# Performance work log

Measured on AMD Instinct MI355X. Metric: run time of the kernel, lower is better.

## Reference

```python
import jax, jax.numpy as jnp
import numpy as np

B, P, C, NOBJ = 64, 24564, 81, 16
THRESHOLD = 0.5
NEG_POS_RATIO = 3
ALPHA = 1.0


def cxcy_to_xy(cxcy):
    # (cx, cy, w, h) -> (x_min, y_min, x_max, y_max)
    return jnp.concatenate([cxcy[..., :2] - cxcy[..., 2:] / 2,
                            cxcy[..., :2] + cxcy[..., 2:] / 2], axis=-1)


def xy_to_cxcy(xy):
    return jnp.concatenate([(xy[..., :2] + xy[..., 2:]) / 2,
                            xy[..., 2:] - xy[..., :2]], axis=-1)


def cxcy_to_gcxgcy(cxcy, priors_cxcy):
    # SSD encoding with variances (10, 5)
    g_cxcy = (cxcy[..., :2] - priors_cxcy[..., :2]) / (priors_cxcy[..., 2:] / 10.0)
    g_wh = jnp.log(cxcy[..., 2:] / priors_cxcy[..., 2:]) * 5.0
    return jnp.concatenate([g_cxcy, g_wh], axis=-1)


def find_jaccard_overlap(set1, set2):
    # set1: [n1, 4] xy, set2: [n2, 4] xy -> IoU [n1, n2]
    lo = jnp.maximum(set1[:, None, :2], set2[None, :, :2])
    hi = jnp.minimum(set1[:, None, 2:], set2[None, :, 2:])
    inter = jnp.prod(jnp.clip(hi - lo, 0.0), axis=-1)
    area1 = jnp.prod(set1[:, 2:] - set1[:, :2], axis=-1)
    area2 = jnp.prod(set2[:, 2:] - set2[:, :2], axis=-1)
    union = area1[:, None] + area2[None, :] - inter
    return inter / union


def setup_inputs() -> dict:
    key = jax.random.key(0)
    k1, k2, k3, k4, k5, k6, k7 = jax.random.split(key, 7)
    predicted_locs = jax.random.normal(k1, (B, P, 4), dtype=jnp.float32)
    predicted_scores = jax.random.normal(k2, (B, P, C), dtype=jnp.float32)
    # valid ground-truth boxes in boundary coords, built from center/size
    ctr = jax.random.uniform(k3, (B, NOBJ, 2), minval=0.2, maxval=0.8)
    wh = jax.random.uniform(k4, (B, NOBJ, 2), minval=0.05, maxval=0.3)
    boxes = jnp.concatenate([ctr - wh / 2, ctr + wh / 2], axis=-1).astype(jnp.float32)
    labels = jax.random.randint(k5, (B, NOBJ), 1, C)  # 0 is background
    pc = jax.random.uniform(k6, (P, 2), minval=0.0, maxval=1.0)
    pwh = jax.random.uniform(k7, (P, 2), minval=0.05, maxval=0.5)
    priors_cxcy = jnp.concatenate([pc, pwh], axis=-1).astype(jnp.float32)
    return {"predicted_locs": predicted_locs, "predicted_scores": predicted_scores,
            "boxes": boxes, "labels": labels, "priors_cxcy": priors_cxcy}


def reference(predicted_locs, predicted_scores, boxes, labels, priors_cxcy):
    priors_xy = cxcy_to_xy(priors_cxcy)

    def match_one(bx, lb):
        # bx: [NOBJ, 4] xy, lb: [NOBJ]
        overlap = find_jaccard_overlap(bx, priors_xy)        # [NOBJ, P]
        ov_per_prior = overlap.max(axis=0)                   # [P]
        obj_per_prior = overlap.argmax(axis=0)               # [P]
        prior_per_obj = overlap.argmax(axis=1)               # [NOBJ]
        # force each object to match its best prior
        obj_per_prior = obj_per_prior.at[prior_per_obj].set(jnp.arange(NOBJ))
        ov_per_prior = ov_per_prior.at[prior_per_obj].set(1.0)
        lab = lb[obj_per_prior]                              # [P]
        lab = jnp.where(ov_per_prior < THRESHOLD, 0, lab)
        tl = cxcy_to_gcxgcy(xy_to_cxcy(bx[obj_per_prior]), priors_cxcy)  # [P, 4]
        return tl, lab

    true_locs, true_classes = jax.vmap(match_one)(boxes, labels)  # [B,P,4], [B,P]

    pos = true_classes != 0                                   # [B, P]
    n_pos = pos.sum(axis=1)                                   # [B]
    total_pos = pos.sum()

    # smooth-L1 (beta=1) over positive priors, mean over elements
    diff = predicted_locs - true_locs
    ad = jnp.abs(diff)
    sl1 = jnp.where(ad < 1.0, 0.5 * diff * diff, ad - 0.5)    # [B, P, 4]
    loc_loss = (sl1 * pos[..., None]).sum() / (total_pos.astype(jnp.float32) * 4.0)

    # per-prior cross-entropy
    logp = jax.nn.log_softmax(predicted_scores, axis=-1)      # [B, P, C]
    ce = -jnp.take_along_axis(logp, true_classes[..., None], axis=-1)[..., 0]  # [B, P]

    conf_loss_pos = jnp.sum(ce * pos)
    conf_loss_neg = jnp.where(pos, 0.0, ce)
    neg_sorted = -jnp.sort(-conf_loss_neg, axis=1)            # descending per image
    ranks = jnp.arange(P)[None, :]
    hard = ranks < (NEG_POS_RATIO * n_pos)[:, None]
    conf_loss_hard_neg = jnp.sum(neg_sorted * hard)

    conf_loss = (conf_loss_hard_neg + conf_loss_pos) / total_pos.astype(jnp.float32)
    return conf_loss + ALPHA * loc_loss
```

## Files before the change

kernel.cpp:

```cpp
#include <hip/hip_runtime.h>
#include <cstdint>
#include <cstddef>

#define B_      64
#define P_      24564
#define C_      81
#define NOBJ_   16
#define CHUNKS_ 96
#define NBLK_   6144
#define TILE_F  1296
#define TILE_F4 324

typedef unsigned long long u64;

__device__ __forceinline__ float smooth_l1(float d){
  float ad = fabsf(d);
  return (ad < 1.0f) ? 0.5f * d * d : ad - 0.5f;
}

__device__ __forceinline__ float iou_pb(float bx0, float by0, float bx1, float by1,
                                        float ba, float px0, float py0,
                                        float px1, float py1, float pa){
  float ix = fminf(bx1, px1) - fmaxf(bx0, px0);
  float iy = fminf(by1, py1) - fmaxf(by0, py0);
  ix = fmaxf(ix, 0.f); iy = fmaxf(iy, 0.f);
  float inter = ix * iy;
  return __fdividef(inter, ba + pa - inter);
}

__device__ __forceinline__ float sl1_row4(const float* sbox, int am, float4 pr, float4 pl){
  float x0 = sbox[am*4+0], y0 = sbox[am*4+1], x1 = sbox[am*4+2], y1 = sbox[am*4+3];
  float cx = (x0 + x1) / 2.f, cy = (y0 + y1) / 2.f;
  float w_ = x1 - x0, h_ = y1 - y0;
  float g0 = (cx - pr.x) / (pr.z / 10.0f);
  float g1 = (cy - pr.y) / (pr.w / 10.0f);
  float g2 = logf(w_ / pr.z) * 5.0f;
  float g3 = logf(h_ / pr.w) * 5.0f;
  return smooth_l1(pl.x - g0) + smooth_l1(pl.y - g1)
       + smooth_l1(pl.z - g2) + smooth_l1(pl.w - g3);
}

__global__ __launch_bounds__(64) void k_main(const float* __restrict__ scores,
                                             const float* __restrict__ priors,
                                             const float* __restrict__ boxes,
                                             const int*   __restrict__ labels,
                                             const float* __restrict__ pred_locs,
                                             float* __restrict__ ce_neg,
                                             u64*   __restrict__ pob,
                                             int*   __restrict__ npos_c,
                                             float* __restrict__ sl1_c,
                                             float* __restrict__ cpos_c,
                                             int*   __restrict__ done){
  __shared__ float sM[2 * TILE_F];
  __shared__ float lmx[256];
  __shared__ int   lam[256];
  __shared__ float sbox[NOBJ_ * 4];
  __shared__ int   slab[NOBJ_];
  const int lane = threadIdx.x;
  const int chk = blockIdx.x, img = blockIdx.y;
  const int blkid = img * CHUNKS_ + chk;
  if (blkid == 0 && lane == 0) *done = 0;

  const int pr0  = chk * 256;
  const int nval = min(256, P_ - pr0);
  sbox[lane] = boxes[img * NOBJ_ * 4 + lane];
  if (lane < NOBJ_) slab[lane] = labels[img * NOBJ_ + lane];

  const size_t brow = (size_t)img * P_ + pr0;
  const float4* g4 = reinterpret_cast<const float4*>(scores + brow * (size_t)C_);
  const int lim = (int)(((size_t)B_ * P_ - brow) * C_ / 4) - 1;

  auto STAGE = [&](int t, float* dst){
    const int b4 = t * TILE_F4;
    #pragma unroll
    for (int k = 0; k < 5; ++k){
      int idx = min(b4 + k * 64 + lane, lim);
      __builtin_amdgcn_global_load_lds(
          (const __attribute__((address_space(1))) void*)(g4 + idx),
          (__attribute__((address_space(3))) void*)(dst + k * 256), 16, 0, 0);
    }
    int idx = min(b4 + 320 + lane, lim);
    if (lane < 4)
      __builtin_amdgcn_global_load_lds(
          (const __attribute__((address_space(1))) void*)(g4 + idx),
          (__attribute__((address_space(3))) void*)(dst + 1280), 16, 0, 0);
  };

  STAGE(0, sM);

  float4 prv[4]; bool pvd[4];
  #pragma unroll
  for (int j = 0; j < 4; ++j){
    int idx = j * 64 + lane;
    pvd[j] = idx < nval;
    prv[j] = reinterpret_cast<const float4*>(priors)[pr0 + (pvd[j] ? idx : 0)];
  }
  float px0[4], py0[4], px1[4], py1[4], pa[4];
  #pragma unroll
  for (int j = 0; j < 4; ++j){
    px0[j] = prv[j].x - prv[j].z * 0.5f;  py0[j] = prv[j].y - prv[j].w * 0.5f;
    px1[j] = prv[j].x + prv[j].z * 0.5f;  py1[j] = prv[j].y + prv[j].w * 0.5f;
    pa[j]  = (px1[j] - px0[j]) * (py1[j] - py0[j]);
  }
  float mx[4]; int am[4];
  #pragma unroll
  for (int j = 0; j < 4; ++j){ mx[j] = -1.f; am[j] = 0; }

  #pragma unroll
  for (int o = 0; o < NOBJ_; ++o){
    float bx0 = sbox[o*4+0], by0 = sbox[o*4+1], bx1 = sbox[o*4+2], by1 = sbox[o*4+3];
    float ba = (bx1 - bx0) * (by1 - by0);
    float bbv = -1.f; int bbi = 0x7FFFFFFF;
    #pragma unroll
    for (int j = 0; j < 4; ++j){
      float v = iou_pb(bx0, by0, bx1, by1, ba, px0[j], py0[j], px1[j], py1[j], pa[j]);
      if (!pvd[j]) v = -2.f;
      int p = pr0 + j * 64 + lane;
      if (v > bbv){ bbv = v; bbi = p; }
      if (v > mx[j]){ mx[j] = v; am[j] = o; }
    }
    #pragma unroll
    for (int off = 32; off; off >>= 1){
      float v2 = __shfl_down(bbv, off);
      int   i2 = __shfl_down(bbi, off);
      if (v2 > bbv || (v2 == bbv && i2 < bbi)){ bbv = v2; bbi = i2; }
    }
    if (lane == 0)
      pob[(size_t)blkid * NOBJ_ + o] =
          ((u64)__float_as_uint(bbv) << 32) | (u64)(0xFFFFFFFFu - (unsigned)bbi);
  }
  #pragma unroll
  for (int j = 0; j < 4; ++j){ lmx[j*64 + lane] = mx[j]; lam[j*64 + lane] = am[j]; }

  int cnt = 0; float sl1 = 0.f, cpos = 0.f;
  const int rr = lane & 15, h = lane >> 4;
  const int rbase = rr * 81 + (h == 0 ? 0 : 1 + 20 * h);

  auto COMPUTE = [&](int t){
    const float* lb = sM + (t & 1) * TILE_F;
    float sa = 0.f, sb = 0.f;
    #pragma unroll
    for (int j = 0; j < 10; ++j){
      sa += __expf(lb[rbase + 2*j]);
      sb += __expf(lb[rbase + 2*j + 1]);
    }
    if (h == 0) sa += __expf(lb[rbase + 20]);
    float sum = sa + sb;
    sum += __shfl_xor(sum, 16);
    sum += __shfl_xor(sum, 32);
    if (h == 0){
      int pl_ = t * 16 + rr;
      if (pl_ < nval){
        size_t row = brow + pl_;
        float lse = __logf(sum);
        float s0  = lb[rr * 81];
        bool pos = lmx[pl_] >= 0.5f;
        ce_neg[row] = pos ? 0.f : fmaxf(lse - s0, 0.f);
        if (pos){
          int a = lam[pl_];
          int lb2 = slab[a];
          cpos += lse - lb[rr * 81 + lb2];
          ++cnt;
          float4 pr  = reinterpret_cast<const float4*>(priors)[pr0 + pl_];
          float4 pl4 = reinterpret_cast<const float4*>(pred_locs)[row];
          sl1 += sl1_row4(sbox, a, pr, pl4);
        }
      }
    }
  };

  for (int t = 0; t < 15; ++t){
    STAGE(t + 1, sM + ((t + 1) & 1) * TILE_F);
    asm volatile("s_waitcnt vmcnt(6)" ::: "memory");
    COMPUTE(t);
  }
  asm volatile("s_waitcnt vmcnt(0)" ::: "memory");
  COMPUTE(15);

  #pragma unroll
  for (int off = 8; off; off >>= 1){
    cnt  += __shfl_down(cnt, off);
    sl1  += __shfl_down(sl1, off);
    cpos += __shfl_down(cpos, off);
  }
  if (lane == 0){
    npos_c[blkid] = cnt; sl1_c[blkid] = sl1; cpos_c[blkid] = cpos;
  }
}

__global__ __launch_bounds__(1024) void k_tail(const float* __restrict__ scores,
                                               const float* __restrict__ priors,
                                               const float* __restrict__ boxes,
                                               const int*   __restrict__ labels,
                                               const float* __restrict__ pred_locs,
                                               const u64*   __restrict__ pob,
                                               const int*   __restrict__ npos_c,
                                               const float* __restrict__ sl1_c,
                                               const float* __restrict__ cpos_c,
                                               float* __restrict__ ce_neg,
                                               int*   __restrict__ npos_img,
                                               float* __restrict__ sl1_img,
                                               float* __restrict__ cpos_img,
                                               float* __restrict__ hard_img,
                                               int*   __restrict__ done,
                                               float* __restrict__ out){
  const int img = blockIdx.x, tid = threadIdx.x;
  const int lane = tid & 63, wid = tid >> 6;
  __shared__ u64   pm[64][NOBJ_];
  __shared__ int   sppo[NOBJ_];
  __shared__ float sbox[NOBJ_ * 4];
  __shared__ int   slab[NOBJ_];
  __shared__ float sredA[96], sredB[96];
  __shared__ int   sredI[96];
  __shared__ int   s_npos;
  __shared__ float s_sl1, s_cpos, s_hard;
  __shared__ int   s_last;

  if (tid < 64) sbox[tid] = boxes[img * 64 + tid];
  if (tid < 16) slab[tid] = labels[img * 16 + tid];
  {
    int o = tid & 15, g = tid >> 4;
    u64 m = pob[(size_t)(img * CHUNKS_ + g) * NOBJ_ + o];
    if (g < 32){
      u64 e = pob[(size_t)(img * CHUNKS_ + 64 + g) * NOBJ_ + o];
      if (e > m) m = e;
    }
    pm[g][o] = m;
  }
  if (tid < 96){
    sredI[tid] = npos_c[img * CHUNKS_ + tid];
    sredA[tid] = sl1_c[img * CHUNKS_ + tid];
    sredB[tid] = cpos_c[img * CHUNKS_ + tid];
  }
  __syncthreads();
  if (tid < 16){
    u64 m = pm[0][tid];
    for (int g = 1; g < 64; ++g) if (pm[g][tid] > m) m = pm[g][tid];
    sppo[tid] = (int)(0xFFFFFFFFu - (unsigned)(m & 0xFFFFFFFFull));
  }
  if (tid == 0){
    int c = 0; float s = 0.f, q = 0.f;
    for (int i = 0; i < 96; ++i){ c += sredI[i]; s += sredA[i]; q += sredB[i]; }
    s_npos = c; s_sl1 = s; s_cpos = q;
  }
  __syncthreads();

  int npd = 0; float sld = 0.f, cpd = 0.f;
  if (wid == 0 && lane < 16){
    int o = lane, p = sppo[o];
    bool is_last = true;
    for (int o2 = o + 1; o2 < 16; ++o2) if (sppo[o2] == p) is_last = false;
    if (is_last){
      float4 pr = reinterpret_cast<const float4*>(priors)[p];
      float px0 = pr.x - pr.z * 0.5f, py0 = pr.y - pr.w * 0.5f;
      float px1 = pr.x + pr.z * 0.5f, py1 = pr.y + pr.w * 0.5f;
      float pa  = (px1 - px0) * (py1 - py0);
      float mxo = -1.f; int amo = 0;
      for (int oo = 0; oo < 16; ++oo){
        float bx0 = sbox[oo*4+0], by0 = sbox[oo*4+1],
              bx1 = sbox[oo*4+2], by1 = sbox[oo*4+3];
        float ba = (bx1 - bx0) * (by1 - by0);
        float v = iou_pb(bx0, by0, bx1, by1, ba, px0, py0, px1, py1, pa);
        if (v > mxo){ mxo = v; amo = oo; }
      }
      bool pos_old = mxo >= 0.5f;
      size_t row = (size_t)img * P_ + p;
      float4 pl4 = reinterpret_cast<const float4*>(pred_locs)[row];
      float sl_new = sl1_row4(sbox, o, pr, pl4);
      int lab_new = slab[o];
      float s_new = scores[row * (size_t)C_ + lab_new];
      if (pos_old){
        float sl_old = sl1_row4(sbox, amo, pr, pl4);
        float s_old  = scores[row * (size_t)C_ + slab[amo]];
        sld = sl_new - sl_old;
        cpd = s_old - s_new;
      } else {
        npd = 1;
        float ce0v = ce_neg[row];
        float s0   = scores[row * (size_t)C_];
        sld = sl_new;
        cpd = ce0v + s0 - s_new;
        ce_neg[row] = 0.f;
      }
    }
  }
  if (wid == 0){
    #pragma unroll
    for (int off = 8; off; off >>= 1){
      npd += __shfl_down(npd, off);
      sld += __shfl_down(sld, off);
      cpd += __shfl_down(cpd, off);
    }
    if (lane == 0){
      s_npos += npd; s_sl1 += sld; s_cpos += cpd;
      npos_img[img] = s_npos; sl1_img[img] = s_sl1; cpos_img[img] = s_cpos;
    }
  }
  __threadfence();
  __syncthreads();

  const int K = 3 * s_npos;
  const float* v = ce_neg + (size_t)img * P_;
  __shared__ int hist[32 * 257];
  __shared__ int histT[256];
  __shared__ unsigned s_prefix;
  __shared__ int s_rem;
  __shared__ float rsum[16];
  const int copy = tid & 31;

  if (K <= 0){
    if (tid == 0) s_hard = 0.f;
    __syncthreads();
  } else if (K >= P_){
    float s = 0.f;
    for (int p = tid; p < P_; p += 1024) s += v[p];
    #pragma unroll
    for (int off = 32; off; off >>= 1) s += __shfl_down(s, off);
    if (lane == 0) rsum[wid] = s;
    __syncthreads();
    if (tid == 0){
      float t = 0.f;
      for (int w = 0; w < 16; ++w) t += rsum[w];
      s_hard = t;
    }
    __syncthreads();
  } else {
    unsigned prefix = 0; int remaining = K;
    for (int shift = 24; shift >= 0; shift -= 8){
      for (int i = tid; i < 32 * 257; i += 1024) hist[i] = 0;
      __syncthreads();
      unsigned hmask = (shift == 24) ? 0u : (0xFFFFFFFFu << (shift + 8));
      for (int p = tid; p < P_; p += 1024){
        unsigned u = __float_as_uint(v[p]);
        if ((u & hmask) == prefix) atomicAdd(&hist[copy * 257 + ((u >> shift) & 255)], 1);
      }
      __syncthreads();
      if (tid < 256){
        int s = 0;
        #pragma unroll
        for (int w = 0; w < 32; ++w) s += hist[w * 257 + tid];
        histT[tid] = s;
      }
      __syncthreads();
      if (wid == 0){
        int a0 = histT[lane*4+0], a1 = histT[lane*4+1],
            a2 = histT[lane*4+2], a3 = histT[lane*4+3];
        int tl = a0 + a1 + a2 + a3;
        int run = tl;
        #pragma unroll
        for (int off = 1; off < 64; off <<= 1){
          int x = __shfl_down(run, off);
          if (lane + off < 64) run += x;
        }
        int E  = run - tl;
        int s3 = E;
        int s2 = s3 + a3;
        int s1 = s2 + a2;
        int s0 = s1 + a1;
        if (s0 < remaining && s0 + a0 >= remaining){ s_prefix = prefix | ((unsigned)(lane*4+0) << shift); s_rem = remaining - s0; }
        if (s1 < remaining && s1 + a1 >= remaining){ s_prefix = prefix | ((unsigned)(lane*4+1) << shift); s_rem = remaining - s1; }
        if (s2 < remaining && s2 + a2 >= remaining){ s_prefix = prefix | ((unsigned)(lane*4+2) << shift); s_rem = remaining - s2; }
        if (s3 < remaining && s3 + a3 >= remaining){ s_prefix = prefix | ((unsigned)(lane*4+3) << shift); s_rem = remaining - s3; }
      }
      __syncthreads();
      prefix = s_prefix;
      remaining = s_rem;
      __syncthreads();
    }
    float tv = __uint_as_float(prefix);
    float sgt = 0.f;
    for (int p = tid; p < P_; p += 1024){
      unsigned u = __float_as_uint(v[p]);
      if (u > prefix) sgt += v[p];
    }
    #pragma unroll
    for (int off = 32; off; off >>= 1) sgt += __shfl_down(sgt, off);
    if (lane == 0) rsum[wid] = sgt;
    __syncthreads();
    if (tid == 0){
      float s = 0.f;
      for (int w = 0; w < 16; ++w) s += rsum[w];
      s_hard = s + (float)remaining * tv;
    }
    __syncthreads();
  }

  if (tid == 0){
    hard_img[img] = s_hard;
    __threadfence();
    int old = atomicAdd(done, 1);
    s_last = (old == B_ - 1) ? 1 : 0;
  }
  __syncthreads();
  if (s_last){
    if (tid == 0) __threadfence();
    __syncthreads();
    float np = 0.f, sl = 0.f, cp = 0.f, hd = 0.f;
    if (tid < 64){
      np = (float)__hip_atomic_load(&npos_img[tid], __ATOMIC_RELAXED, __HIP_MEMORY_SCOPE_AGENT);
      sl = __hip_atomic_load(&sl1_img[tid],  __ATOMIC_RELAXED, __HIP_MEMORY_SCOPE_AGENT);
      cp = __hip_atomic_load(&cpos_img[tid], __ATOMIC_RELAXED, __HIP_MEMORY_SCOPE_AGENT);
      hd = __hip_atomic_load(&hard_img[tid], __ATOMIC_RELAXED, __HIP_MEMORY_SCOPE_AGENT);
    }
    if (wid == 0){
      #pragma unroll
      for (int off = 32; off; off >>= 1){
        np += __shfl_down(np, off);
        sl += __shfl_down(sl, off);
        cp += __shfl_down(cp, off);
        hd += __shfl_down(hd, off);
      }
      if (lane == 0){
        out[0] = (hd + cp) / np + sl / (np * 4.0f);
      }
    }
  }
}

extern "C" void kernel_launch(void* const* d_in, const int* in_sizes, int n_in,
                              void* d_out, int out_size, void* d_ws, size_t ws_size,
                              hipStream_t stream){
  const float* pred_locs = (const float*)d_in[0];
  const float* scores    = (const float*)d_in[1];
  const float* boxes     = (const float*)d_in[2];
  const int*   labels    = (const int*)d_in[3];
  const float* priors    = (const float*)d_in[4];

  const size_t BP = (size_t)B_ * P_;
  char* w = (char*)d_ws;
  float* ce_neg = (float*)w;
  u64*   pob    = (u64*)(w + BP * 4);
  char*  w2 = w + BP * 4 + (size_t)NBLK_ * NOBJ_ * 8;
  int*   npos_c = (int*)  w2;
  float* sl1_c  = (float*)(w2 + NBLK_ * 4);
  float* cpos_c = (float*)(w2 + NBLK_ * 8);
  char*  w3 = w2 + NBLK_ * 12;
  int*   npos_img = (int*)  w3;
  float* sl1_img  = (float*)(w3 + 256);
  float* cpos_img = (float*)(w3 + 512);
  float* hard_img = (float*)(w3 + 768);
  int*   done     = (int*)  (w3 + 1024);

  dim3 g1(CHUNKS_, B_);
  k_main<<<g1, 64, 0, stream>>>(scores, priors, boxes, labels, pred_locs,
                                ce_neg, pob, npos_c, sl1_c, cpos_c, done);

  k_tail<<<B_, 1024, 0, stream>>>(scores, priors, boxes, labels, pred_locs,
                                  pob, npos_c, sl1_c, cpos_c, ce_neg,
                                  npos_img, sl1_img, cpos_img, hard_img,
                                  done, (float*)d_out);
}
```

Measured before the change: 182.6 us.

## Load score rows directly into registers instead of staging through LDS

Drops the global_load_lds double-buffered shared-memory staging of score tiles. Each lane now reads its 20-21 logits straight from global memory into register buffers, prefetched two tiles ahead. The positive-class logit is re-read from global memory. This cuts LDS use and the explicit waitcnt handling, but lanes issue strided, less coalesced scalar loads and register pressure rises, and the runtime-indexed double buffers may spill to scratch.

```diff
diff --git a/kernel.cpp b/kernel.cpp
--- a/kernel.cpp
+++ b/kernel.cpp
@@ -8,8 +8,6 @@
 #define NOBJ_   16
 #define CHUNKS_ 96
 #define NBLK_   6144
-#define TILE_F  1296
-#define TILE_F4 324
 
 typedef unsigned long long u64;
 
@@ -51,7 +49,6 @@
                                              float* __restrict__ sl1_c,
                                              float* __restrict__ cpos_c,
                                              int*   __restrict__ done){
-  __shared__ float sM[2 * TILE_F];
   __shared__ float lmx[256];
   __shared__ int   lam[256];
   __shared__ float sbox[NOBJ_ * 4];
@@ -67,26 +64,19 @@
   if (lane < NOBJ_) slab[lane] = labels[img * NOBJ_ + lane];
 
   const size_t brow = (size_t)img * P_ + pr0;
-  const float4* g4 = reinterpret_cast<const float4*>(scores + brow * (size_t)C_);
-  const int lim = (int)(((size_t)B_ * P_ - brow) * C_ / 4) - 1;
-
-  auto STAGE = [&](int t, float* dst){
-    const int b4 = t * TILE_F4;
-    #pragma unroll
-    for (int k = 0; k < 5; ++k){
-      int idx = min(b4 + k * 64 + lane, lim);
-      __builtin_amdgcn_global_load_lds(
-          (const __attribute__((address_space(1))) void*)(g4 + idx),
-          (__attribute__((address_space(3))) void*)(dst + k * 256), 16, 0, 0);
-    }
-    int idx = min(b4 + 320 + lane, lim);
-    if (lane < 4)
-      __builtin_amdgcn_global_load_lds(
-          (const __attribute__((address_space(1))) void*)(g4 + idx),
-          (__attribute__((address_space(3))) void*)(dst + 1280), 16, 0, 0);
+  const int rr = lane & 15, h = lane >> 4;
+  const int off0 = (h == 0) ? 0 : 1 + 20 * h;
+
+  float bufA[21], bufB[21];
+  auto LD = [&](int t, float* d){
+    int pl = min(t * 16 + rr, nval - 1);
+    const float* src = scores + (brow + (size_t)pl) * (size_t)C_ + off0;
+    #pragma unroll
+    for (int c = 0; c < 20; ++c) d[c] = src[c];
+    d[20] = (h == 0) ? src[20] : -1.0e30f;
   };
 
-  STAGE(0, sM);
+  LD(0, bufA);
 
   float4 prv[4]; bool pvd[4];
   #pragma unroll
@@ -133,19 +123,15 @@
   for (int j = 0; j < 4; ++j){ lmx[j*64 + lane] = mx[j]; lam[j*64 + lane] = am[j]; }
 
   int cnt = 0; float sl1 = 0.f, cpos = 0.f;
-  const int rr = lane & 15, h = lane >> 4;
-  const int rbase = rr * 81 + (h == 0 ? 0 : 1 + 20 * h);
-
-  auto COMPUTE = [&](int t){
-    const float* lb = sM + (t & 1) * TILE_F;
+
+  auto CMP = [&](int t, const float* d){
     float sa = 0.f, sb = 0.f;
     #pragma unroll
-    for (int j = 0; j < 10; ++j){
-      sa += __expf(lb[rbase + 2*j]);
-      sb += __expf(lb[rbase + 2*j + 1]);
-    }
-    if (h == 0) sa += __expf(lb[rbase + 20]);
-    float sum = sa + sb;
+    for (int c = 0; c < 10; ++c){
+      sa += __expf(d[2*c]);
+      sb += __expf(d[2*c + 1]);
+    }
+    float sum = sa + sb + __expf(d[20]);
     sum += __shfl_xor(sum, 16);
     sum += __shfl_xor(sum, 32);
     if (h == 0){
@@ -153,13 +139,13 @@
       if (pl_ < nval){
         size_t row = brow + pl_;
         float lse = __logf(sum);
-        float s0  = lb[rr * 81];
+        float s0  = d[0];
         bool pos = lmx[pl_] >= 0.5f;
         ce_neg[row] = pos ? 0.f : fmaxf(lse - s0, 0.f);
         if (pos){
           int a = lam[pl_];
-          int lb2 = slab[a];
-          cpos += lse - lb[rr * 81 + lb2];
+          int cls = slab[a];
+          cpos += lse - scores[row * (size_t)C_ + cls];
           ++cnt;
           float4 pr  = reinterpret_cast<const float4*>(priors)[pr0 + pl_];
           float4 pl4 = reinterpret_cast<const float4*>(pred_locs)[row];
@@ -169,13 +155,12 @@
     }
   };
 
-  for (int t = 0; t < 15; ++t){
-    STAGE(t + 1, sM + ((t + 1) & 1) * TILE_F);
-    asm volatile("s_waitcnt vmcnt(6)" ::: "memory");
-    COMPUTE(t);
-  }
-  asm volatile("s_waitcnt vmcnt(0)" ::: "memory");
-  COMPUTE(15);
+  LD(1, bufB);
+  for (int t = 0; t < 16; ++t){
+    float* curb = (t & 1) ? bufB : bufA;
+    CMP(t, curb);
+    if (t + 2 < 16) LD(t + 2, curb);
+  }
 
   #pragma unroll
   for (int off = 8; off; off >>= 1){
```

New measurement: 184.9 us. No clear change (+1.2%).
